# Kernel tuning notes

Hardware: AMD Instinct MI355X
Metric: run time of the kernel (lower is better)

Reference implementation:

```python
import jax, jax.numpy as jnp
import numpy as np
from jax import lax

# Module hyperparameters (init_kwargs)
B, T, F, H = 512, 256, 64, 128
D = F + H            # decoder LSTMCell width = input_dim + hidden_rnn
OUT_DIM = 32         # output_dim (survival horizon steps)
RISKS = 2
NEG = -1e10


def lstm_cell(x, h, c, Wih, Whh):
    # PyTorch gate order: i, f, g, o; bias=False
    g = x @ Wih.T + h @ Whh.T
    i, f, gg, o = jnp.split(g, 4, axis=-1)
    c = jax.nn.sigmoid(f) * c + jax.nn.sigmoid(i) * jnp.tanh(gg)
    h = jax.nn.sigmoid(o) * jnp.tanh(c)
    return h, c


def setup_inputs() -> dict:
    key = jax.random.key(0)
    ks = jax.random.split(key, 12)
    rn = lambda k, shp, fan: jax.random.normal(k, shp, jnp.float32) * (1.0 / np.sqrt(fan))
    return {
        "x": jax.random.normal(ks[0], (B, T, F), jnp.float32),
        # encoder LSTM (1 layer, bias=False)
        "W_ih_emb": rn(ks[1], (4 * H, F), F),
        "W_hh_emb": rn(ks[2], (4 * H, H), H),
        # longitudinal head: Linear(H -> F)
        "W_long": rn(ks[3], (F, H), H),
        "b_long": jnp.zeros((F,), jnp.float32),
        # attention head: Linear(F+H -> 1)
        "W_att": rn(ks[4], (1, D), D),
        "b_att": jnp.zeros((1,), jnp.float32),
        # per-risk cause-specific LSTMCell (bias=False) and Linear(D -> 1)
        "W_ih_cs": rn(ks[5], (RISKS, 4 * D, D), D),
        "W_hh_cs": rn(ks[6], (RISKS, 4 * D, D), D),
        "W_cs": rn(ks[7], (RISKS, 1, D), D),
        "b_cs": jnp.zeros((RISKS, 1), jnp.float32),
    }


def _forward(x, W_ih_emb, W_hh_emb, W_long, b_long, W_att, b_att,
             W_ih_cs, W_hh_cs, W_cs, b_cs):
    inputmask = jnp.abs(x).sum(2) == 0                      # [B,T]
    last_obs = (~inputmask).sum(axis=1) - 1                 # [B]

    # encoder LSTM over time
    def enc_step(carry, xt):
        h, c = carry
        h, c = lstm_cell(xt, h, c, W_ih_emb, W_hh_emb)
        return (h, c), h

    h0 = jnp.zeros((x.shape[0], H), x.dtype)
    _, hs = lax.scan(enc_step, (h0, h0), x.transpose(1, 0, 2))
    hidden = hs.transpose(1, 0, 2)                          # [B,T,H]

    long_pred = hidden @ W_long.T + b_long                  # [B,T,F]

    x_last = x[jnp.arange(x.shape[0]), last_obs]            # [B,F]
    concat = jnp.concatenate(
        [hidden, jnp.broadcast_to(x_last[:, None, :], (x.shape[0], x.shape[1], F))], -1)
    scores = (concat @ W_att.T + b_att)[..., 0]             # [B,T]

    idx = jnp.arange(x.shape[1])[None, :]
    scores = jnp.where(idx >= last_obs[:, None], NEG, scores)
    att = jax.nn.softmax(scores, axis=1)
    att = jnp.where((last_obs > 0)[:, None], att, 0.0)      # rows with last_obs==0 zeroed

    hidden_att = jnp.einsum('bt,bth->bh', att, hidden)      # [B,H]
    ha = jnp.concatenate([hidden_att, x_last], 1)           # [B,D]

    state0 = (lax.stop_gradient(ha), lax.stop_gradient(ha))  # .detach() on init state
    rs = jnp.arange(OUT_DIM * RISKS) % RISKS                # k-major, r-minor loop order

    def dec_step(carry, r):
        h, c = carry
        h, c = lstm_cell(ha, h, c, W_ih_cs[r], W_hh_cs[r])
        out = jax.nn.sigmoid(h @ W_cs[r].T + b_cs[r])       # [B,1]
        return (h, c), out

    _, outs = lax.scan(dec_step, state0, rs)                # [steps,B,1]
    outcomes = jax.nn.softmax(outs[..., 0].T, axis=-1)      # [B, OUT_DIM*RISKS]
    parts = tuple(outcomes[:, i * OUT_DIM:(i + 1) * OUT_DIM] for i in range(RISKS))
    return (long_pred,) + parts


def reference(x, W_ih_emb, W_hh_emb, W_long, b_long, W_att, b_att,
              W_ih_cs, W_hh_cs, W_cs, b_cs):
    return _forward(x, W_ih_emb, W_hh_emb, W_long, b_long, W_att, b_att,
                    W_ih_cs, W_hh_cs, W_cs, b_cs)
```

## Files before the change

kernel.cpp:

```cpp
#include <hip/hip_runtime.h>
#include <stdint.h>

#define DEV __device__ __forceinline__
typedef unsigned short u16; typedef unsigned int u32; typedef unsigned long long u64;
typedef __attribute__((ext_vector_type(8))) short s8v;
typedef __attribute__((ext_vector_type(4))) float f4v;

#define Bb 512
#define Tt 256
#define Ff 64
#define Hh 128
#define Dd 192
#define L2E  1.4426950408889634f
#define L2E2 2.8853900817779268f

DEV u16 f2bf(float f){ u32 u = __builtin_bit_cast(u32, f); u32 r = (u + 0x7fffu + ((u>>16)&1u)) >> 16; return (u16)r; }
DEV float sigm(float x){ return __builtin_amdgcn_rcpf(1.0f + __expf(-x)); }
DEV float ex2(float x){ float r; asm("v_exp_f32 %0, %1" : "=v"(r) : "v"(x)); return r; }
DEV float sig2n(float y){ return __builtin_amdgcn_rcpf(1.0f + ex2(y)); }
DEV float th2 (float y){ return 1.0f - 2.0f*__builtin_amdgcn_rcpf(1.0f + ex2(y)); }
DEV u32 cvtpk(float lo, float hi){ u32 d; asm("v_cvt_pk_bf16_f32 %0, %1, %2" : "=v"(d) : "v"(lo), "v"(hi)); return d; }
DEV float blo(u32 q){ return __builtin_bit_cast(float, q<<16); }
DEV float bhi(u32 q){ return __builtin_bit_cast(float, q & 0xffff0000u); }

DEV f4v mfma16(s8v a, s8v b, f4v c){ return __builtin_amdgcn_mfma_f32_16x16x32_bf16(a, b, c, 0, 0, 0); }

DEV void barrier_lds(){ asm volatile("s_waitcnt lgkmcnt(0)\n\ts_barrier" ::: "memory"); }

DEV int hxe2(int k, int c){ return (k>>5)*512 + (((k>>3)&3)*16 + c)*8 + (k&7); }

DEV s8v pack8s(const float* p, float sc){
  const float4 a = *(const float4*)p; const float4 b = *(const float4*)(p+4);
  s8v r; r[0]=(short)f2bf(a.x*sc); r[1]=(short)f2bf(a.y*sc); r[2]=(short)f2bf(a.z*sc); r[3]=(short)f2bf(a.w*sc);
  r[4]=(short)f2bf(b.x*sc); r[5]=(short)f2bf(b.y*sc); r[6]=(short)f2bf(b.z*sc); r[7]=(short)f2bf(b.w*sc); return r;
}
DEV s8v pack8(const float* p){ return pack8s(p, 1.0f); }
DEV u32 pk2(float a, float b){ return (u32)f2bf(a) | ((u32)f2bf(b)<<16); }

__global__ __launch_bounds__(64) void prelim_k(const float* __restrict__ x,
    const float* __restrict__ Watt, const float* __restrict__ batt,
    float* __restrict__ xlast, float* __restrict__ c0, int* __restrict__ lastobs)
{
  int b = blockIdx.x, tid = threadIdx.x;
  int cnt = 0;
  for (int it = 0; it < 4; ++it){
    int t = it*64 + tid;
    const float4* p = (const float4*)(x + ((size_t)b*Tt + t)*Ff);
    float s = 0.0f;
    #pragma unroll
    for (int q = 0; q < 16; ++q){ float4 v = p[q]; s += fabsf(v.x)+fabsf(v.y)+fabsf(v.z)+fabsf(v.w); }
    u64 m = __ballot(s != 0.0f);
    cnt += __popcll(m);
  }
  int last = cnt - 1;
  int li = (last < 0) ? (Tt-1) : last;
  float xl = x[((size_t)b*Tt + li)*Ff + tid];
  xlast[b*Ff + tid] = xl;
  float p = xl * Watt[Hh + tid];
  for (int off = 32; off; off >>= 1) p += __shfl_down(p, off);
  if (tid == 0){ c0[b] = (p + batt[0]) * L2E; lastobs[b] = last; }
}

__global__ __launch_bounds__(256) void prep_wd_k(const float* __restrict__ Whhcs,
    const float* __restrict__ Wihcs, u16* __restrict__ Wd, u16* __restrict__ WdIH)
{
  int idx = blockIdx.x*256 + threadIdx.x;
  int j = idx & 7, lane = (idx>>3)&63;
  int f = idx>>9;
  int kt = f % 6; int mtr = f/6;
  int mt = mtr % 48, r = mtr/48;
  int ut = mt>>2, g = mt&3;
  int row = g*Dd + ut*16 + (lane&15);
  int k = kt*32 + (lane>>4)*8 + j;
  float sc = (g == 2) ? L2E2 : -L2E;
  size_t src = ((size_t)r*768 + row)*Dd + k;
  Wd[idx]   = f2bf(Whhcs[src] * sc);
  WdIH[idx] = f2bf(Wihcs[src] * sc);
}

__global__ __launch_bounds__(64) void xw_k(const u16* __restrict__ WdIH,
    const float* __restrict__ ha, u16* __restrict__ xwg)
{
  int lane = threadIdx.x, l15 = lane&15, l4 = lane>>4;
  int cg = blockIdx.x & 3, rm = blockIdx.x >> 2;
  s8v af[6];
  #pragma unroll
  for (int kt=0;kt<6;++kt) af[kt] = *(const s8v*)(WdIH + (size_t)(rm*6+kt)*512 + lane*8);
  #pragma unroll
  for (int ct=0; ct<8; ++ct){
    int c = cg*128 + ct*16 + l15;
    f4v a = {0,0,0,0};
    #pragma unroll
    for (int kt=0;kt<6;++kt){
      s8v b = pack8(ha + (size_t)c*Dd + kt*32 + l4*8);
      a = mfma16(af[kt], b, a);
    }
    int bg = cg*8 + ct;
    int base = bg*24576 + rm*256 + l15*16 + l4*4;
    *(u32*)&xwg[base]   = pk2(a[0], a[1]);
    *(u32*)&xwg[base+2] = pk2(a[2], a[3]);
  }
}

__global__ __launch_bounds__(512)
__attribute__((amdgpu_waves_per_eu(2,2)))
void enc_k(
    const float* __restrict__ x, const float* __restrict__ Whh, const float* __restrict__ Wih,
    const float* __restrict__ Wlong, const float* __restrict__ blong, const float* __restrict__ Watt,
    const float* __restrict__ xlast, const float* __restrict__ c0v, const int* __restrict__ lastobs,
    float* __restrict__ lp_out, float* __restrict__ ha)
{
  __shared__ __align__(16) u16 hx[2][3072];
  __shared__ float sarr[2][16];
  const int tid = threadIdx.x, wid = tid>>6, lane = tid&63, l15 = lane&15, l4 = lane>>4;
  const int b0 = blockIdx.x*16;
  const int xrow = tid>>5, xc2 = (tid&31)*2;

  s8v wf[4][6];
  #pragma unroll
  for (int mt = 0; mt < 4; ++mt){
    int gate = mt*Hh + wid*16 + l15;
    float sc = (mt == 2) ? L2E2 : -L2E;
    #pragma unroll
    for (int kt = 0; kt < 6; ++kt){
      int k0 = kt*32 + l4*8;
      if (kt < 4) wf[mt][kt] = pack8s(Whh + (size_t)gate*Hh + k0, sc);
      else        wf[mt][kt] = pack8s(Wih + (size_t)gate*Ff + (k0 - Hh), sc);
    }
  }
  s8v wfx[6];
  {
    s8v z = {0,0,0,0,0,0,0,0};
    #pragma unroll
    for (int kt = 0; kt < 6; ++kt) wfx[kt] = z;
    if (wid < 4){
      int f = wid*16 + l15;
      #pragma unroll
      for (int kt = 0; kt < 4; ++kt) wfx[kt] = pack8(Wlong + (size_t)f*Hh + kt*32 + l4*8);
    } else if (wid == 4 && l15 == 0){
      #pragma unroll
      for (int kt = 0; kt < 4; ++kt) wfx[kt] = pack8s(Watt + kt*32 + l4*8, L2E);
    }
  }
  float bl[4] = {0,0,0,0};
  if (wid < 4){
    #pragma unroll
    for (int j = 0; j < 4; ++j) bl[j] = blong[wid*16 + l4*4 + j];
  }
  const int   lastb = lastobs[b0 + l15];
  const float c0b   = c0v[b0 + l15];

  const int he0 = hxe2(wid*16 + l4*4, l15);
  const int xe0 = hxe2(Hh + xc2, xrow);
  float* lpb = lp_out + ((size_t)(b0+l15)*Tt)*Ff + wid*16 + l4*4;

  ((u64*)hx[0])[tid] = 0ull;
  {
    float2 xv = *(const float2*)(x + ((size_t)(b0+xrow)*Tt + 0)*Ff + xc2);
    *(u32*)&hx[0][xe0] = cvtpk(xv.x, xv.y);
  }
  float2 xa = *(const float2*)(x + ((size_t)(b0+xrow)*Tt + 1)*Ff + xc2);
  float2 xb;
  __syncthreads();

  float cst[4] = {0,0,0,0}, hp[4] = {0,0,0,0}, hpp[4] = {0,0,0,0};
  float accA[4] = {0,0,0,0}, mrun = -3.0e38f, zrun = 0.0f;

#define ENC_STEP(T_, CURB_, NXTB_, XC_, XN_) { \
    const int t = (T_); \
    s8v bf[6]; \
    _Pragma("unroll") \
    for (int kt = 0; kt < 6; ++kt) \
      bf[kt] = *(const s8v*)&hx[CURB_][kt*512 + lane*8]; \
    { int tp = t + 2; if (tp > Tt-1) tp = Tt-1; \
      XN_ = *(const float2*)(x + ((size_t)(b0+xrow)*Tt + tp)*Ff + xc2); } \
    f4v acc0 = {0,0,0,0}, acc1 = {0,0,0,0}, acc2 = {0,0,0,0}, acc3 = {0,0,0,0}, accx = {0,0,0,0}; \
    _Pragma("unroll") \
    for (int kt = 0; kt < 6; ++kt){ \
      acc0 = mfma16(wf[0][kt], bf[kt], acc0); \
      acc1 = mfma16(wf[1][kt], bf[kt], acc1); \
      acc2 = mfma16(wf[2][kt], bf[kt], acc2); \
      acc3 = mfma16(wf[3][kt], bf[kt], acc3); \
    } \
    if (wid < 5){ \
      _Pragma("unroll") \
      for (int kt = 0; kt < 6; ++kt) accx = mfma16(wfx[kt], bf[kt], accx); \
    } \
    if (wid == 4 && l4 == 0) sarr[NXTB_][l15] = accx[0] + c0b; \
    float hnew[4]; \
    _Pragma("unroll") \
    for (int j = 0; j < 4; ++j){ \
      float si = sig2n(acc0[j]), sf = sig2n(acc1[j]); \
      float tg = th2(acc2[j]),   so = sig2n(acc3[j]); \
      float cn = sf*cst[j] + si*tg; \
      cst[j] = cn; \
      hnew[j] = so * th2(cn * L2E2); \
    } \
    if (t >= 2){ \
      float sv = sarr[CURB_][l15]; \
      if (t-2 < lastb){ \
        float mn = fmaxf(mrun, sv); \
        float sc = ex2(mrun - mn); \
        float e  = ex2(sv - mn); \
        zrun = zrun*sc + e; \
        _Pragma("unroll") \
        for (int j = 0; j < 4; ++j) accA[j] = accA[j]*sc + e*hpp[j]; \
        mrun = mn; \
      } \
    } \
    _Pragma("unroll") \
    for (int j = 0; j < 4; ++j){ hpp[j] = hp[j]; hp[j] = hnew[j]; } \
    { u32 plo = cvtpk(hnew[0], hnew[1]), phi = cvtpk(hnew[2], hnew[3]); \
      *(u64*)&hx[NXTB_][he0] = (u64)plo | ((u64)phi<<32); } \
    if (t < Tt-1) *(u32*)&hx[NXTB_][xe0] = cvtpk(XC_.x, XC_.y); \
    if (wid < 4 && t >= 1){ \
      float4 v; v.x = accx[0]+bl[0]; v.y = accx[1]+bl[1]; v.z = accx[2]+bl[2]; v.w = accx[3]+bl[3]; \
      *(float4*)(lpb + (size_t)(t-1)*Ff) = v; \
    } \
    barrier_lds(); }

  for (int tp2 = 0; tp2 < 128; ++tp2){
    ENC_STEP(2*tp2,   0, 1, xa, xb)
    ENC_STEP(2*tp2+1, 1, 0, xb, xa)
  }
#undef ENC_STEP

  {
    if (254 < lastb){
      float sv = sarr[0][l15];
      float mn = fmaxf(mrun, sv);
      float sc = ex2(mrun - mn);
      float e  = ex2(sv - mn);
      zrun = zrun*sc + e;
      #pragma unroll
      for (int j = 0; j < 4; ++j) accA[j] = accA[j]*sc + e*hpp[j];
      mrun = mn;
    }
    s8v bfE[4];
    #pragma unroll
    for (int kt = 0; kt < 4; ++kt)
      bfE[kt] = *(const s8v*)&hx[0][kt*512 + lane*8];
    if (wid < 4){
      f4v accx = {0,0,0,0};
      #pragma unroll
      for (int kt = 0; kt < 4; ++kt) accx = mfma16(wfx[kt], bfE[kt], accx);
      float4 v; v.x = accx[0]+bl[0]; v.y = accx[1]+bl[1]; v.z = accx[2]+bl[2]; v.w = accx[3]+bl[3];
      *(float4*)(lpb + (size_t)(Tt-1)*Ff) = v;
    }
    float inv = (zrun > 0.0f) ? __builtin_amdgcn_rcpf(zrun) : 0.0f;
    #pragma unroll
    for (int j = 0; j < 4; ++j)
      ha[(size_t)(b0 + l15)*Dd + wid*16 + l4*4 + j] = accA[j]*inv;
    __syncthreads();
    for (int q = tid; q < 16*Ff; q += 512){
      int r2 = q >> 6, f = q & 63;
      ha[(size_t)(b0 + r2)*Dd + Hh + f] = xlast[(b0 + r2)*Ff + f];
    }
  }
}

__global__ __launch_bounds__(768)
void dec_k(const float* __restrict__ ha,
    const u16* __restrict__ Wd, const u16* __restrict__ xwg,
    const float* __restrict__ Wcs, const float* __restrict__ bcs, float* __restrict__ outs)
{
  __shared__ __align__(16) u16 hx[2][3072];
  __shared__ float red[2][12][16];
  const int tid = threadIdx.x, wid = tid>>6, lane = tid&63, l15 = lane&15, l4 = lane>>4;
  const int b0 = blockIdx.x*16;

  {
    int k = (tid>>4)*4, c = tid&15;
    float4 v = *(const float4*)(ha + (size_t)(b0+c)*Dd + k);
    int e = hxe2(k, c);
    *(u32*)&hx[0][e]   = cvtpk(v.x, v.y);
    *(u32*)&hx[0][e+2] = cvtpk(v.z, v.w);
  }
  s8v wreg[2][4][6];
  #pragma unroll
  for (int r = 0; r < 2; ++r)
    #pragma unroll
    for (int g = 0; g < 4; ++g)
      #pragma unroll
      for (int kt = 0; kt < 6; ++kt)
        wreg[r][g][kt] = *(const s8v*)(Wd + (size_t)(((r*48 + wid*4 + g)*6) + kt)*512 + lane*8);
  u32 xwr[2][4][2];
  #pragma unroll
  for (int r = 0; r < 2; ++r)
    #pragma unroll
    for (int g = 0; g < 4; ++g){
      int base = blockIdx.x*24576 + (r*48 + wid*4 + g)*256 + l15*16 + l4*4;
      u64 q = *(const u64*)&xwg[base];
      xwr[r][g][0] = (u32)q; xwr[r][g][1] = (u32)(q>>32);
    }
  const int u0 = wid*16 + l4*4;
  float cst[4], wcs0[4], wcs1[4];
  #pragma unroll
  for (int j = 0; j < 4; ++j){
    cst[j]  = ha[(size_t)(b0+l15)*Dd + u0 + j];
    wcs0[j] = Wcs[u0 + j];
    wcs1[j] = Wcs[Dd + u0 + j];
  }
  const float bc0 = bcs[0], bc1 = bcs[1];
  const int he0 = hxe2(u0, l15);
  __syncthreads();

#define DEC_STEP(R_, CURB_, NXTB_, WCS_, BC_, S_) { \
    s8v bf[6]; \
    _Pragma("unroll") \
    for (int kt = 0; kt < 6; ++kt) bf[kt] = *(const s8v*)&hx[CURB_][kt*512 + lane*8]; \
    f4v a0, a1, a2, a3; \
    { u32 lo, hi; \
      lo = xwr[R_][0][0]; hi = xwr[R_][0][1]; a0[0]=blo(lo); a0[1]=bhi(lo); a0[2]=blo(hi); a0[3]=bhi(hi); \
      lo = xwr[R_][1][0]; hi = xwr[R_][1][1]; a1[0]=blo(lo); a1[1]=bhi(lo); a1[2]=blo(hi); a1[3]=bhi(hi); \
      lo = xwr[R_][2][0]; hi = xwr[R_][2][1]; a2[0]=blo(lo); a2[1]=bhi(lo); a2[2]=blo(hi); a2[3]=bhi(hi); \
      lo = xwr[R_][3][0]; hi = xwr[R_][3][1]; a3[0]=blo(lo); a3[1]=bhi(lo); a3[2]=blo(hi); a3[3]=bhi(hi); } \
    _Pragma("unroll") \
    for (int kt = 0; kt < 6; ++kt){ \
      a0 = mfma16(wreg[R_][0][kt], bf[kt], a0); \
      a1 = mfma16(wreg[R_][1][kt], bf[kt], a1); \
      a2 = mfma16(wreg[R_][2][kt], bf[kt], a2); \
      a3 = mfma16(wreg[R_][3][kt], bf[kt], a3); } \
    float part = 0.0f, hn[4]; \
    _Pragma("unroll") \
    for (int j = 0; j < 4; ++j){ \
      float si = sig2n(a0[j]), sf = sig2n(a1[j]); \
      float tg = th2(a2[j]),   so = sig2n(a3[j]); \
      float cn = sf*cst[j] + si*tg; \
      cst[j] = cn; \
      hn[j] = so * th2(cn * L2E2); \
      part += hn[j] * WCS_[j]; } \
    { u32 plo = cvtpk(hn[0], hn[1]), phi = cvtpk(hn[2], hn[3]); \
      *(u64*)&hx[NXTB_][he0] = (u64)plo | ((u64)phi<<32); } \
    part += __shfl_xor(part, 16); part += __shfl_xor(part, 32); \
    if (l4 == 0) red[(S_)&1][wid][l15] = part; \
    barrier_lds(); \
    if (tid < 16){ \
      float ss = BC_; \
      _Pragma("unroll") \
      for (int q = 0; q < 12; ++q) ss += red[(S_)&1][q][tid]; \
      outs[(S_)*Bb + b0 + tid] = sigm(ss); } }

  for (int sp = 0; sp < 32; ++sp){
    DEC_STEP(0, 0, 1, wcs0, bc0, sp*2)
    DEC_STEP(1, 1, 0, wcs1, bc1, sp*2+1)
  }
#undef DEC_STEP
}

__global__ __launch_bounds__(256) void fin_k(const float* __restrict__ outs, float* __restrict__ dout)
{
  int row = blockIdx.x*256 + threadIdx.x;
  float v[64]; float mx = -3.0e38f;
  #pragma unroll
  for (int s = 0; s < 64; ++s){ v[s] = outs[s*Bb + row]; mx = fmaxf(mx, v[s]); }
  float sum = 0.0f;
  #pragma unroll
  for (int s = 0; s < 64; ++s){ v[s] = __expf(v[s] - mx); sum += v[s]; }
  float inv = __builtin_amdgcn_rcpf(sum);
  float* p0 = dout + (size_t)Bb*Tt*Ff;
  float* p1 = p0 + Bb*32;
  #pragma unroll
  for (int j = 0; j < 32; ++j) p0[row*32 + j] = v[j]*inv;
  #pragma unroll
  for (int j = 0; j < 32; ++j) p1[row*32 + j] = v[32 + j]*inv;
}

extern "C" void kernel_launch(void* const* d_in, const int* in_sizes, int n_in,
                              void* d_out, int out_size, void* d_ws, size_t ws_size,
                              hipStream_t stream)
{
  const float* x      = (const float*)d_in[0];
  const float* Wih    = (const float*)d_in[1];
  const float* Whh    = (const float*)d_in[2];
  const float* Wlong  = (const float*)d_in[3];
  const float* blong  = (const float*)d_in[4];
  const float* Watt   = (const float*)d_in[5];
  const float* batt   = (const float*)d_in[6];
  const float* Wihcs  = (const float*)d_in[7];
  const float* Whhcs  = (const float*)d_in[8];
  const float* Wcs    = (const float*)d_in[9];
  const float* bcs    = (const float*)d_in[10];
  float* out = (float*)d_out;
  char* ws = (char*)d_ws;

  float* xlast   = (float*)ws;
  float* c0      = (float*)(ws + 131072);
  int*   lastobs = (int*)  (ws + 133120);
  float* ha      = (float*)(ws + 135168);
  u16*   Wd      = (u16*)  (ws + 528384);
  u16*   WdIH    = (u16*)  (ws + 1118208);
  u16*   xwg     = (u16*)  (ws + 1708032);
  float* outs    = (float*)(ws + 3280896);

  prep_wd_k<<<1152, 256, 0, stream>>>(Whhcs, Wihcs, Wd, WdIH);
  prelim_k<<<Bb, 64, 0, stream>>>(x, Watt, batt, xlast, c0, lastobs);
  enc_k<<<32, 512, 0, stream>>>(x, Whh, Wih, Wlong, blong, Watt, xlast, c0, lastobs, out, ha);
  xw_k<<<384, 64, 0, stream>>>(WdIH, ha, xwg);
  dec_k<<<32, 768, 0, stream>>>(ha, Wd, xwg, Wcs, bcs, outs);
  fin_k<<<2, 256, 0, stream>>>(outs, out);
}
```

Before: 645.4 us.

## Split decoder weights across registers, LDS and streamed global loads for occupancy

```diff
diff --git a/kernel.cpp b/kernel.cpp
--- a/kernel.cpp
+++ b/kernel.cpp
@@ -24,7 +24,6 @@
 DEV float bhi(u32 q){ return __builtin_bit_cast(float, q & 0xffff0000u); }
 
 DEV f4v mfma16(s8v a, s8v b, f4v c){ return __builtin_amdgcn_mfma_f32_16x16x32_bf16(a, b, c, 0, 0, 0); }
-
 DEV void barrier_lds(){ asm volatile("s_waitcnt lgkmcnt(0)\n\ts_barrier" ::: "memory"); }
 
 DEV int hxe2(int k, int c){ return (k>>5)*512 + (((k>>3)&3)*16 + c)*8 + (k&7); }
@@ -259,12 +258,14 @@
   }
 }
 
-__global__ __launch_bounds__(768)
-void dec_k(const float* __restrict__ ha,
-    const u16* __restrict__ Wd, const u16* __restrict__ xwg,
-    const float* __restrict__ Wcs, const float* __restrict__ bcs, float* __restrict__ outs)
+__global__ __launch_bounds__(768, 3)
+void dec_k(const float* __restrict__ ha, const u16* __restrict__ Wd,
+    const u16* __restrict__ xwg, const float* __restrict__ Wcs,
+    const float* __restrict__ bcs, float* __restrict__ outs)
 {
   __shared__ __align__(16) u16 hx[2][3072];
+  __shared__ __align__(16) u16 w1[12*4*2*512];
+  __shared__ __align__(16) u16 xwl[2*48*256];
   __shared__ float red[2][12][16];
   const int tid = threadIdx.x, wid = tid>>6, lane = tid&63, l15 = lane&15, l4 = lane>>4;
   const int b0 = blockIdx.x*16;
@@ -276,23 +277,28 @@
     *(u32*)&hx[0][e]   = cvtpk(v.x, v.y);
     *(u32*)&hx[0][e+2] = cvtpk(v.z, v.w);
   }
-  s8v wreg[2][4][6];
-  #pragma unroll
-  for (int r = 0; r < 2; ++r)
-    #pragma unroll
-    for (int g = 0; g < 4; ++g)
-      #pragma unroll
-      for (int kt = 0; kt < 6; ++kt)
-        wreg[r][g][kt] = *(const s8v*)(Wd + (size_t)(((r*48 + wid*4 + g)*6) + kt)*512 + lane*8);
-  u32 xwr[2][4][2];
-  #pragma unroll
-  for (int r = 0; r < 2; ++r)
-    #pragma unroll
-    for (int g = 0; g < 4; ++g){
-      int base = blockIdx.x*24576 + (r*48 + wid*4 + g)*256 + l15*16 + l4*4;
-      u64 q = *(const u64*)&xwg[base];
-      xwr[r][g][0] = (u32)q; xwr[r][g][1] = (u32)(q>>32);
-    }
+  {
+    const u16* src = xwg + (size_t)blockIdx.x*24576;
+    #pragma unroll
+    for (int i = 0; i < 4; ++i){
+      int off = (i*768 + tid)*8;
+      *(s8v*)&xwl[off] = *(const s8v*)(src + off);
+    }
+  }
+  #pragma unroll
+  for (int i = 0; i < 8; ++i){
+    int off = (i*768 + tid)*8;
+    int chunk = off>>9, inner = off&511;
+    int mtg = chunk>>1, kt = chunk&1;
+    *(s8v*)&w1[off] = *(const s8v*)(Wd + (size_t)((48 + mtg)*6 + kt)*512 + inner);
+  }
+  s8v wreg[4][4];
+  #pragma unroll
+  for (int g = 0; g < 4; ++g)
+    #pragma unroll
+    for (int kt = 0; kt < 4; ++kt)
+      wreg[g][kt] = *(const s8v*)(Wd + (size_t)((wid*4 + g)*6 + kt)*512 + lane*8);
+
   const int u0 = wid*16 + l4*4;
   float cst[4], wcs0[4], wcs1[4];
   #pragma unroll
@@ -305,25 +311,29 @@
   const int he0 = hxe2(u0, l15);
   __syncthreads();
 
-#define DEC_STEP(R_, CURB_, NXTB_, WCS_, BC_, S_) { \
-    s8v bf[6]; \
-    _Pragma("unroll") \
-    for (int kt = 0; kt < 6; ++kt) bf[kt] = *(const s8v*)&hx[CURB_][kt*512 + lane*8]; \
-    f4v a0, a1, a2, a3; \
-    { u32 lo, hi; \
-      lo = xwr[R_][0][0]; hi = xwr[R_][0][1]; a0[0]=blo(lo); a0[1]=bhi(lo); a0[2]=blo(hi); a0[3]=bhi(hi); \
-      lo = xwr[R_][1][0]; hi = xwr[R_][1][1]; a1[0]=blo(lo); a1[1]=bhi(lo); a1[2]=blo(hi); a1[3]=bhi(hi); \
-      lo = xwr[R_][2][0]; hi = xwr[R_][2][1]; a2[0]=blo(lo); a2[1]=bhi(lo); a2[2]=blo(hi); a2[3]=bhi(hi); \
-      lo = xwr[R_][3][0]; hi = xwr[R_][3][1]; a3[0]=blo(lo); a3[1]=bhi(lo); a3[2]=blo(hi); a3[3]=bhi(hi); } \
-    _Pragma("unroll") \
-    for (int kt = 0; kt < 6; ++kt){ \
-      a0 = mfma16(wreg[R_][0][kt], bf[kt], a0); \
-      a1 = mfma16(wreg[R_][1][kt], bf[kt], a1); \
-      a2 = mfma16(wreg[R_][2][kt], bf[kt], a2); \
-      a3 = mfma16(wreg[R_][3][kt], bf[kt], a3); } \
+  s8v sA[4], sB[4], sC[4];
+#define LDG(BUF_, R_, KT_) { \
+    _Pragma("unroll") for (int g_ = 0; g_ < 4; ++g_) \
+      BUF_[g_] = *(const s8v*)(Wd + (size_t)(((R_)*48 + wid*4 + g_)*6 + (KT_))*512 + lane*8); }
+
+#define XWI(R_) { \
+    u32 lo, hi; u64 q; \
+    q = *(const u64*)&xwl[((R_)*48 + wid*4 + 0)*256 + l15*16 + l4*4]; \
+    lo = (u32)q; hi = (u32)(q>>32); a0[0]=blo(lo); a0[1]=bhi(lo); a0[2]=blo(hi); a0[3]=bhi(hi); \
+    q = *(const u64*)&xwl[((R_)*48 + wid*4 + 1)*256 + l15*16 + l4*4]; \
+    lo = (u32)q; hi = (u32)(q>>32); a1[0]=blo(lo); a1[1]=bhi(lo); a1[2]=blo(hi); a1[3]=bhi(hi); \
+    q = *(const u64*)&xwl[((R_)*48 + wid*4 + 2)*256 + l15*16 + l4*4]; \
+    lo = (u32)q; hi = (u32)(q>>32); a2[0]=blo(lo); a2[1]=bhi(lo); a2[2]=blo(hi); a2[3]=bhi(hi); \
+    q = *(const u64*)&xwl[((R_)*48 + wid*4 + 3)*256 + l15*16 + l4*4]; \
+    lo = (u32)q; hi = (u32)(q>>32); a3[0]=blo(lo); a3[1]=bhi(lo); a3[2]=blo(hi); a3[3]=bhi(hi); }
+
+#define M4(W0_, W1_, W2_, W3_, BF_) { \
+    a0 = mfma16(W0_, BF_, a0); a1 = mfma16(W1_, BF_, a1); \
+    a2 = mfma16(W2_, BF_, a2); a3 = mfma16(W3_, BF_, a3); }
+
+#define CELLS(WCS_, NXTB_, PAR_, BC_, S_) { \
     float part = 0.0f, hn[4]; \
-    _Pragma("unroll") \
-    for (int j = 0; j < 4; ++j){ \
+    _Pragma("unroll") for (int j = 0; j < 4; ++j){ \
       float si = sig2n(a0[j]), sf = sig2n(a1[j]); \
       float tg = th2(a2[j]),   so = sig2n(a3[j]); \
       float cn = sf*cst[j] + si*tg; \
@@ -333,19 +343,63 @@
     { u32 plo = cvtpk(hn[0], hn[1]), phi = cvtpk(hn[2], hn[3]); \
       *(u64*)&hx[NXTB_][he0] = (u64)plo | ((u64)phi<<32); } \
     part += __shfl_xor(part, 16); part += __shfl_xor(part, 32); \
-    if (l4 == 0) red[(S_)&1][wid][l15] = part; \
+    if (l4 == 0) red[PAR_][wid][l15] = part; \
     barrier_lds(); \
     if (tid < 16){ \
       float ss = BC_; \
-      _Pragma("unroll") \
-      for (int q = 0; q < 12; ++q) ss += red[(S_)&1][q][tid]; \
+      _Pragma("unroll") for (int q = 0; q < 12; ++q) ss += red[PAR_][q][tid]; \
       outs[(S_)*Bb + b0 + tid] = sigm(ss); } }
 
+  LDG(sA, 0, 4); LDG(sB, 0, 5); LDG(sC, 1, 2);
+
   for (int sp = 0; sp < 32; ++sp){
-    DEC_STEP(0, 0, 1, wcs0, bc0, sp*2)
-    DEC_STEP(1, 1, 0, wcs1, bc1, sp*2+1)
-  }
-#undef DEC_STEP
+    {
+      f4v a0, a1, a2, a3;
+      XWI(0)
+      #pragma unroll
+      for (int kt = 0; kt < 4; ++kt){
+        s8v bf = *(const s8v*)&hx[0][kt*512 + lane*8];
+        M4(wreg[0][kt], wreg[1][kt], wreg[2][kt], wreg[3][kt], bf)
+      }
+      { s8v bf = *(const s8v*)&hx[0][4*512 + lane*8];
+        M4(sA[0], sA[1], sA[2], sA[3], bf) }
+      LDG(sA, 1, 3);
+      { s8v bf = *(const s8v*)&hx[0][5*512 + lane*8];
+        M4(sB[0], sB[1], sB[2], sB[3], bf) }
+      LDG(sB, 1, 4);
+      CELLS(wcs0, 1, 0, bc0, sp*2)
+    }
+    {
+      f4v a0, a1, a2, a3;
+      XWI(1)
+      #pragma unroll
+      for (int kt = 0; kt < 2; ++kt){
+        s8v bf = *(const s8v*)&hx[1][kt*512 + lane*8];
+        s8v q0 = *(const s8v*)&w1[((wid*4+0)*2+kt)*512 + lane*8];
+        s8v q1 = *(const s8v*)&w1[((wid*4+1)*2+kt)*512 + lane*8];
+        s8v q2 = *(const s8v*)&w1[((wid*4+2)*2+kt)*512 + lane*8];
+        s8v q3 = *(const s8v*)&w1[((wid*4+3)*2+kt)*512 + lane*8];
+        M4(q0, q1, q2, q3, bf)
+      }
+      { s8v bf = *(const s8v*)&hx[1][2*512 + lane*8];
+        M4(sC[0], sC[1], sC[2], sC[3], bf) }
+      LDG(sC, 1, 5);
+      { s8v bf = *(const s8v*)&hx[1][3*512 + lane*8];
+        M4(sA[0], sA[1], sA[2], sA[3], bf) }
+      LDG(sA, 0, 4);
+      { s8v bf = *(const s8v*)&hx[1][4*512 + lane*8];
+        M4(sB[0], sB[1], sB[2], sB[3], bf) }
+      LDG(sB, 0, 5);
+      { s8v bf = *(const s8v*)&hx[1][5*512 + lane*8];
+        M4(sC[0], sC[1], sC[2], sC[3], bf) }
+      LDG(sC, 1, 2);
+      CELLS(wcs1, 0, 1, bc1, sp*2+1)
+    }
+  }
+#undef LDG
+#undef XWI
+#undef M4
+#undef CELLS
 }
 
 __global__ __launch_bounds__(256) void fin_k(const float* __restrict__ outs, float* __restrict__ dout)
```

Measured after the change: 590.6 us. 1.09x faster.

## Stream decoder weights through LDS ring via async global-to-LDS DMA

Applied to the files above, without the earlier changes.

```diff
diff --git a/kernel.cpp b/kernel.cpp
--- a/kernel.cpp
+++ b/kernel.cpp
@@ -24,8 +24,12 @@
 DEV float bhi(u32 q){ return __builtin_bit_cast(float, q & 0xffff0000u); }
 
 DEV f4v mfma16(s8v a, s8v b, f4v c){ return __builtin_amdgcn_mfma_f32_16x16x32_bf16(a, b, c, 0, 0, 0); }
-
 DEV void barrier_lds(){ asm volatile("s_waitcnt lgkmcnt(0)\n\ts_barrier" ::: "memory"); }
+
+DEV void dma16(const void* g, void* l){
+  __builtin_amdgcn_global_load_lds((const __attribute__((address_space(1))) void*)g,
+                                   (__attribute__((address_space(3))) void*)l, 16, 0, 0);
+}
 
 DEV int hxe2(int k, int c){ return (k>>5)*512 + (((k>>3)&3)*16 + c)*8 + (k&7); }
 
@@ -259,12 +263,13 @@
   }
 }
 
-__global__ __launch_bounds__(768)
-void dec_k(const float* __restrict__ ha,
-    const u16* __restrict__ Wd, const u16* __restrict__ xwg,
-    const float* __restrict__ Wcs, const float* __restrict__ bcs, float* __restrict__ outs)
+__global__ __launch_bounds__(768, 3)
+void dec_k(const float* __restrict__ ha, const u16* __restrict__ Wd,
+    const u16* __restrict__ xwg, const float* __restrict__ Wcs,
+    const float* __restrict__ bcs, float* __restrict__ outs)
 {
   __shared__ __align__(16) u16 hx[2][3072];
+  __shared__ __align__(16) u16 wstr[12*12*512];
   __shared__ float red[2][12][16];
   const int tid = threadIdx.x, wid = tid>>6, lane = tid&63, l15 = lane&15, l4 = lane>>4;
   const int b0 = blockIdx.x*16;
@@ -276,14 +281,6 @@
     *(u32*)&hx[0][e]   = cvtpk(v.x, v.y);
     *(u32*)&hx[0][e+2] = cvtpk(v.z, v.w);
   }
-  s8v wreg[2][4][6];
-  #pragma unroll
-  for (int r = 0; r < 2; ++r)
-    #pragma unroll
-    for (int g = 0; g < 4; ++g)
-      #pragma unroll
-      for (int kt = 0; kt < 6; ++kt)
-        wreg[r][g][kt] = *(const s8v*)(Wd + (size_t)(((r*48 + wid*4 + g)*6) + kt)*512 + lane*8);
   u32 xwr[2][4][2];
   #pragma unroll
   for (int r = 0; r < 2; ++r)
@@ -303,27 +300,35 @@
   }
   const float bc0 = bcs[0], bc1 = bcs[1];
   const int he0 = hxe2(u0, l15);
+  u16* const wring = &wstr[wid*12*512];
   __syncthreads();
 
-#define DEC_STEP(R_, CURB_, NXTB_, WCS_, BC_, S_) { \
-    s8v bf[6]; \
-    _Pragma("unroll") \
-    for (int kt = 0; kt < 6; ++kt) bf[kt] = *(const s8v*)&hx[CURB_][kt*512 + lane*8]; \
-    f4v a0, a1, a2, a3; \
-    { u32 lo, hi; \
-      lo = xwr[R_][0][0]; hi = xwr[R_][0][1]; a0[0]=blo(lo); a0[1]=bhi(lo); a0[2]=blo(hi); a0[3]=bhi(hi); \
-      lo = xwr[R_][1][0]; hi = xwr[R_][1][1]; a1[0]=blo(lo); a1[1]=bhi(lo); a1[2]=blo(hi); a1[3]=bhi(hi); \
-      lo = xwr[R_][2][0]; hi = xwr[R_][2][1]; a2[0]=blo(lo); a2[1]=bhi(lo); a2[2]=blo(hi); a2[3]=bhi(hi); \
-      lo = xwr[R_][3][0]; hi = xwr[R_][3][1]; a3[0]=blo(lo); a3[1]=bhi(lo); a3[2]=blo(hi); a3[3]=bhi(hi); } \
-    _Pragma("unroll") \
-    for (int kt = 0; kt < 6; ++kt){ \
-      a0 = mfma16(wreg[R_][0][kt], bf[kt], a0); \
-      a1 = mfma16(wreg[R_][1][kt], bf[kt], a1); \
-      a2 = mfma16(wreg[R_][2][kt], bf[kt], a2); \
-      a3 = mfma16(wreg[R_][3][kt], bf[kt], a3); } \
+#define WSRC(R_, KT_, G_) (Wd + (size_t)(((R_)*48 + wid*4 + (G_))*6 + (KT_))*512 + lane*8)
+#define ISSUE_G(RT_, KTT_, KTG_) { \
+    dma16(WSRC(RT_, KTT_, 0), wring + ((4*(KTG_)+0)%12)*512); \
+    dma16(WSRC(RT_, KTT_, 1), wring + ((4*(KTG_)+1)%12)*512); \
+    dma16(WSRC(RT_, KTT_, 2), wring + ((4*(KTG_)+2)%12)*512); \
+    dma16(WSRC(RT_, KTT_, 3), wring + ((4*(KTG_)+3)%12)*512); }
+#define GRP(CURB_, KTG_) { \
+    asm volatile("s_waitcnt vmcnt(8)" ::: "memory"); \
+    s8v q0 = *(const s8v*)(wring + ((4*(KTG_)+0)%12)*512 + lane*8); \
+    s8v q1 = *(const s8v*)(wring + ((4*(KTG_)+1)%12)*512 + lane*8); \
+    s8v q2 = *(const s8v*)(wring + ((4*(KTG_)+2)%12)*512 + lane*8); \
+    s8v q3 = *(const s8v*)(wring + ((4*(KTG_)+3)%12)*512 + lane*8); \
+    s8v bf = *(const s8v*)&hx[CURB_][(KTG_)*512 + lane*8]; \
+    a0 = mfma16(q0, bf, a0); a1 = mfma16(q1, bf, a1); \
+    a2 = mfma16(q2, bf, a2); a3 = mfma16(q3, bf, a3); }
+
+#define XWI(R_) { \
+    u32 lo, hi; \
+    lo = xwr[R_][0][0]; hi = xwr[R_][0][1]; a0[0]=blo(lo); a0[1]=bhi(lo); a0[2]=blo(hi); a0[3]=bhi(hi); \
+    lo = xwr[R_][1][0]; hi = xwr[R_][1][1]; a1[0]=blo(lo); a1[1]=bhi(lo); a1[2]=blo(hi); a1[3]=bhi(hi); \
+    lo = xwr[R_][2][0]; hi = xwr[R_][2][1]; a2[0]=blo(lo); a2[1]=bhi(lo); a2[2]=blo(hi); a2[3]=bhi(hi); \
+    lo = xwr[R_][3][0]; hi = xwr[R_][3][1]; a3[0]=blo(lo); a3[1]=bhi(lo); a3[2]=blo(hi); a3[3]=bhi(hi); }
+
+#define CELLS(WCS_, NXTB_, PAR_, BC_, S_) { \
     float part = 0.0f, hn[4]; \
-    _Pragma("unroll") \
-    for (int j = 0; j < 4; ++j){ \
+    _Pragma("unroll") for (int j = 0; j < 4; ++j){ \
       float si = sig2n(a0[j]), sf = sig2n(a1[j]); \
       float tg = th2(a2[j]),   so = sig2n(a3[j]); \
       float cn = sf*cst[j] + si*tg; \
@@ -333,18 +338,36 @@
     { u32 plo = cvtpk(hn[0], hn[1]), phi = cvtpk(hn[2], hn[3]); \
       *(u64*)&hx[NXTB_][he0] = (u64)plo | ((u64)phi<<32); } \
     part += __shfl_xor(part, 16); part += __shfl_xor(part, 32); \
-    if (l4 == 0) red[(S_)&1][wid][l15] = part; \
+    if (l4 == 0) red[PAR_][wid][l15] = part; \
     barrier_lds(); \
     if (tid < 16){ \
       float ss = BC_; \
-      _Pragma("unroll") \
-      for (int q = 0; q < 12; ++q) ss += red[(S_)&1][q][tid]; \
+      _Pragma("unroll") for (int q = 0; q < 12; ++q) ss += red[PAR_][q][tid]; \
       outs[(S_)*Bb + b0 + tid] = sigm(ss); } }
 
+#define DEC_STEP(R_, RN_, CURB_, NXTB_, WCS_, BC_, PAR_, S_) { \
+    f4v a0, a1, a2, a3; \
+    XWI(R_) \
+    GRP(CURB_, 0) ISSUE_G(R_,  3, 0) \
+    GRP(CURB_, 1) ISSUE_G(R_,  4, 1) \
+    GRP(CURB_, 2) ISSUE_G(R_,  5, 2) \
+    GRP(CURB_, 3) ISSUE_G(RN_, 0, 3) \
+    GRP(CURB_, 4) ISSUE_G(RN_, 1, 4) \
+    GRP(CURB_, 5) ISSUE_G(RN_, 2, 5) \
+    CELLS(WCS_, NXTB_, PAR_, BC_, S_) }
+
+  ISSUE_G(0, 0, 0); ISSUE_G(0, 1, 1); ISSUE_G(0, 2, 2);
+
   for (int sp = 0; sp < 32; ++sp){
-    DEC_STEP(0, 0, 1, wcs0, bc0, sp*2)
-    DEC_STEP(1, 1, 0, wcs1, bc1, sp*2+1)
-  }
+    DEC_STEP(0, 1, 0, 1, wcs0, bc0, 0, sp*2)
+    DEC_STEP(1, 0, 1, 0, wcs1, bc1, 1, sp*2+1)
+  }
+  asm volatile("s_waitcnt vmcnt(0)" ::: "memory");
+#undef WSRC
+#undef ISSUE_G
+#undef GRP
+#undef XWI
+#undef CELLS
 #undef DEC_STEP
 }
 
```

New measurement: 546.8 us. -15.3%, faster.
